# Optimization experiments

Measured on AMD Instinct MI355X. Metric: run time of the kernel, lower is better.

## Reference

```python
import jax, jax.numpy as jnp
import numpy as np

SCALE = 1.0

def _sq_dist(p0, p1):
    # p0: [B,N,3], p1: [B,M,3] -> [B,N,M] squared euclidean distances
    n0 = jnp.sum(p0 * p0, axis=-1)  # [B,N]
    n1 = jnp.sum(p1 * p1, axis=-1)  # [B,M]
    inner = jnp.einsum('bnd,bmd->bnm', p0, p1)  # [B,N,M]
    return n0[:, :, None] + n1[:, None, :] - 2.0 * inner

def setup_inputs() -> dict:
    key = jax.random.key(0)
    k0, k1 = jax.random.split(key)
    template = jax.random.normal(k0, (4, 8192, 3), dtype=jnp.float32)
    source = jax.random.normal(k1, (4, 8192, 3), dtype=jnp.float32)
    return {"template": template, "source": source}

def reference(template, source):
    p0 = template / SCALE
    p1 = source / SCALE
    d = _sq_dist(p0, p1)  # [B,N,M]
    # nearest neighbor in each direction, averaged over points
    d01 = jnp.mean(jnp.min(d, axis=2), axis=1)  # template -> source, [B]
    d10 = jnp.mean(jnp.min(d, axis=1), axis=1)  # source -> template, [B]
    return d01 + d10  # per-batch chamfer distance (reduction='none')
```

## Files before the change

kernel.cpp:

```cpp
#include <hip/hip_runtime.h>


typedef __bf16 bf16x8 __attribute__((ext_vector_type(8)));
typedef float  f32x16 __attribute__((ext_vector_type(16)));

constexpr int B     = 4;
constexpr int NPTS  = 8192;
constexpr int BLOCK = 256;
constexpr int QPW   = 64;
constexpr int QPB   = 256;
constexpr int QBLKS = NPTS / QPB;
constexpr int CH    = 4;
constexpr int CPTS  = NPTS / CH;
constexpr int SPTS  = 512;
constexpr int NPASS = CPTS / SPTS;
constexpr int TPP   = SPTS / 32;
constexpr size_t KEYBYTES = (size_t)2 * B * NPTS * sizeof(unsigned);

__device__ inline unsigned key_of(float f) {
    unsigned b = __float_as_uint(f);
    return b ^ (unsigned)(((int)b >> 31) | (int)0x80000000u);
}
__device__ inline float float_of(unsigned k) {
    unsigned b = (k & 0x80000000u) ? (k ^ 0x80000000u) : ~k;
    return __uint_as_float(b);
}

__global__ __launch_bounds__(BLOCK) void chamfer_prep(
    const float* __restrict__ tpl, const float* __restrict__ src,
    bf16x8* __restrict__ efrag)
{
    const int pt  = blockIdx.x * BLOCK + threadIdx.x;
    const int c   = blockIdx.y;
    const int b   = c & (B - 1);
    const int dir = c >> 2;
    const float* db = (dir == 0 ? src : tpl) + (size_t)b * NPTS * 3;

    float x = db[3 * pt], y = db[3 * pt + 1], z = db[3 * pt + 2];
    float n = -0.5f * (x * x + y * y + z * z);
    __bf16 hx = (__bf16)x, hy = (__bf16)y, hz = (__bf16)z;
    __bf16 lx = (__bf16)(x - (float)hx);
    __bf16 ly = (__bf16)(y - (float)hy);
    __bf16 lz = (__bf16)(z - (float)hz);
    __bf16 nh = (__bf16)n;
    __bf16 nl = (__bf16)(n - (float)nh);
    const __bf16 zb = (__bf16)0.0f;

    bf16x8 e0 = {hx, hy, hz, lx, ly, lz, hx, hy};
    bf16x8 e1 = {hz, nh, nl, lx, ly, lz, zb, zb};
    size_t base = ((size_t)c * NPTS + pt) * 2;
    efrag[base]     = e0;
    efrag[base + 1] = e1;
}

__global__ __launch_bounds__(BLOCK, 4) void chamfer_sweep(
    const float* __restrict__ tpl, const float* __restrict__ src,
    const bf16x8* __restrict__ efrag,
    unsigned* __restrict__ keys)
{
    __shared__ bf16x8 sbuf[SPTS * 2];

    const int tid = threadIdx.x;
    const int l   = tid & 63;
    const int w   = tid >> 6;
    const int h   = l >> 5;
    const int r32 = l & 31;
    const int c   = blockIdx.z;
    const int b   = c & (B - 1);
    const int dir = c >> 2;
    const float* q = (dir == 0 ? tpl : src) + (size_t)b * NPTS * 3;
    const int qbase  = blockIdx.x * QPB + w * QPW;
    const int cstart = blockIdx.y * CPTS;

    const __bf16 one = (__bf16)1.0f, zb = (__bf16)0.0f;
    bf16x8 fa[2];
    #pragma unroll
    for (int f = 0; f < 2; ++f) {
        int qi = qbase + f * 32 + r32;
        float x = q[3 * qi], y = q[3 * qi + 1], z = q[3 * qi + 2];
        __bf16 hx = (__bf16)x, hy = (__bf16)y, hz = (__bf16)z;
        __bf16 lx = (__bf16)(x - (float)hx);
        __bf16 ly = (__bf16)(y - (float)hy);
        __bf16 lz = (__bf16)(z - (float)hz);
        if (h == 0) fa[f] = (bf16x8){hx, hy, hz, hx, hy, hz, lx, ly};
        else        fa[f] = (bf16x8){lz, one, one, lx, ly, lz, zb, zb};
    }

    f32x16 best0, best1, zc;
    #pragma unroll
    for (int r = 0; r < 16; ++r) { best0[r] = -3.4e38f; best1[r] = -3.4e38f; zc[r] = 0.0f; }

    const bf16x8* eb = efrag + ((size_t)c * NPTS + cstart) * 2;
    bf16x8 rg[4];
    #pragma unroll
    for (int i = 0; i < 4; ++i) rg[i] = eb[tid + i * 256];

    for (int p = 0; p < NPASS; ++p) {
        __syncthreads();
        #pragma unroll
        for (int i = 0; i < 4; ++i) sbuf[tid + i * 256] = rg[i];
        if (p + 1 < NPASS) {
            const bf16x8* ebn = eb + (size_t)(p + 1) * SPTS * 2;
            #pragma unroll
            for (int i = 0; i < 4; ++i) rg[i] = ebn[tid + i * 256];
        }
        __syncthreads();

        #pragma unroll 2
        for (int t = 0; t < TPP; ++t) {
            bf16x8 bv = sbuf[t * 64 + r32 * 2 + h];
            f32x16 d0 = __builtin_amdgcn_mfma_f32_32x32x16_bf16(fa[0], bv, zc, 0, 0, 0);
            f32x16 d1 = __builtin_amdgcn_mfma_f32_32x32x16_bf16(fa[1], bv, zc, 0, 0, 0);
            #pragma unroll
            for (int r = 0; r < 16; ++r) {
                best0[r] = fmaxf(best0[r], d0[r]);
                best1[r] = fmaxf(best1[r], d1[r]);
            }
        }
    }

    #pragma unroll
    for (int m = 1; m < 32; m <<= 1) {
        #pragma unroll
        for (int r = 0; r < 16; ++r) {
            best0[r] = fmaxf(best0[r], __shfl_xor(best0[r], m, 64));
            best1[r] = fmaxf(best1[r], __shfl_xor(best1[r], m, 64));
        }
    }
    if (r32 == 0) {
        unsigned* kz = keys + (size_t)c * NPTS;
        #pragma unroll
        for (int r = 0; r < 16; ++r) {
            int row = (r & 3) + 8 * (r >> 2) + 4 * h;
            atomicMax(&kz[qbase + row],      key_of(best0[r]));
            atomicMax(&kz[qbase + 32 + row], key_of(best1[r]));
        }
    }
}

__global__ __launch_bounds__(256) void chamfer_final(
    const float* __restrict__ tpl, const float* __restrict__ src,
    const unsigned* __restrict__ keys, float* __restrict__ out)
{
    __shared__ float red[256];
    const int z   = blockIdx.x >> 4;
    const int seg = blockIdx.x & 15;
    const float* qc = (z < B ? tpl : src) + (size_t)(z & (B - 1)) * NPTS * 3;

    float s = 0.f;
    const int lo = seg * (NPTS / 16);
    for (int i = lo + threadIdx.x; i < lo + NPTS / 16; i += 256) {
        float md = float_of(keys[(size_t)z * NPTS + i]);
        float x = qc[3 * i], y = qc[3 * i + 1], zz = qc[3 * i + 2];
        s += fmaf(md, -2.0f, x * x + y * y + zz * zz);
    }
    red[threadIdx.x] = s;
    __syncthreads();
    #pragma unroll
    for (int off = 128; off > 0; off >>= 1) {
        if (threadIdx.x < off) red[threadIdx.x] += red[threadIdx.x + off];
        __syncthreads();
    }
    if (threadIdx.x == 0)
        atomicAdd(&out[z & (B - 1)], red[0] * (1.0f / NPTS));
}

extern "C" void kernel_launch(void* const* d_in, const int* in_sizes, int n_in,
                              void* d_out, int out_size, void* d_ws, size_t ws_size,
                              hipStream_t stream) {
    const float* tpl = (const float*)d_in[0];
    const float* src = (const float*)d_in[1];
    float* out = (float*)d_out;
    unsigned* keys = (unsigned*)d_ws;
    bf16x8* efrag  = (bf16x8*)((char*)d_ws + KEYBYTES);

    hipMemsetAsync(d_ws, 0x00, KEYBYTES, stream);
    hipMemsetAsync(d_out, 0x00, (size_t)B * sizeof(float), stream);
    chamfer_prep <<<dim3(NPTS / BLOCK, 2 * B), BLOCK, 0, stream>>>(tpl, src, efrag);
    chamfer_sweep<<<dim3(QBLKS, CH, 2 * B),    BLOCK, 0, stream>>>(tpl, src, efrag, keys);
    chamfer_final<<<B * 16 * 2, 256, 0, stream>>>(tpl, src, keys, out);
}
```

Baseline: 41.94 us.

## Double-buffer sweep LDS via async global_load_lds and fold memsets into prep

The sweep kernel now streams each pass of encoded points straight from global memory into a double-buffered LDS tile using global_load_lds. This drops the register staging copy and one of the two barriers per pass. The MFMA loop is restructured to process two tiles per iteration and chain the max reductions. The two hipMemsetAsync calls are replaced by zeroing keys and output inside the prep kernel, and the final kernel uses one block per batch-direction instead of 16 segments. The final reduction therefore runs with much less parallelism, and correctness depends on the barrier waiting for the async LDS loads.

```diff
diff --git a/kernel.cpp b/kernel.cpp
--- a/kernel.cpp
+++ b/kernel.cpp
@@ -1,4 +1,5 @@
 #include <hip/hip_runtime.h>
+#include <stdint.h>
 
 
 typedef __bf16 bf16x8 __attribute__((ext_vector_type(8)));
@@ -15,6 +16,7 @@
 constexpr int SPTS  = 512;
 constexpr int NPASS = CPTS / SPTS;
 constexpr int TPP   = SPTS / 32;
+constexpr int PASSBYTES = SPTS * 2 * 16;
 constexpr size_t KEYBYTES = (size_t)2 * B * NPTS * sizeof(unsigned);
 
 __device__ inline unsigned key_of(float f) {
@@ -26,15 +28,25 @@
     return __uint_as_float(b);
 }
 
+__device__ inline void gload_lds16(const void* g, void* l) {
+    __builtin_amdgcn_global_load_lds(
+        (const __attribute__((address_space(1))) uint32_t*)g,
+        (__attribute__((address_space(3))) uint32_t*)l, 16, 0, 0);
+}
+
 __global__ __launch_bounds__(BLOCK) void chamfer_prep(
     const float* __restrict__ tpl, const float* __restrict__ src,
-    bf16x8* __restrict__ efrag)
+    bf16x8* __restrict__ efrag,
+    unsigned* __restrict__ keys, float* __restrict__ out)
 {
     const int pt  = blockIdx.x * BLOCK + threadIdx.x;
     const int c   = blockIdx.y;
     const int b   = c & (B - 1);
     const int dir = c >> 2;
     const float* db = (dir == 0 ? src : tpl) + (size_t)b * NPTS * 3;
+
+    keys[(size_t)c * NPTS + pt] = 0u;
+    if (blockIdx.x == 0 && c == 0 && threadIdx.x < B) out[threadIdx.x] = 0.f;
 
     float x = db[3 * pt], y = db[3 * pt + 1], z = db[3 * pt + 2];
     float n = -0.5f * (x * x + y * y + z * z);
@@ -46,11 +58,9 @@
     __bf16 nl = (__bf16)(n - (float)nh);
     const __bf16 zb = (__bf16)0.0f;
 
-    bf16x8 e0 = {hx, hy, hz, lx, ly, lz, hx, hy};
-    bf16x8 e1 = {hz, nh, nl, lx, ly, lz, zb, zb};
     size_t base = ((size_t)c * NPTS + pt) * 2;
-    efrag[base]     = e0;
-    efrag[base + 1] = e1;
+    efrag[base]     = (bf16x8){hx, hy, hz, lx, ly, lz, hx, hy};
+    efrag[base + 1] = (bf16x8){hz, nh, nl, lx, ly, lz, zb, zb};
 }
 
 __global__ __launch_bounds__(BLOCK, 4) void chamfer_sweep(
@@ -58,7 +68,7 @@
     const bf16x8* __restrict__ efrag,
     unsigned* __restrict__ keys)
 {
-    __shared__ bf16x8 sbuf[SPTS * 2];
+    __shared__ bf16x8 sbuf[2][SPTS * 2];
 
     const int tid = threadIdx.x;
     const int l   = tid & 63;
@@ -69,8 +79,14 @@
     const int b   = c & (B - 1);
     const int dir = c >> 2;
     const float* q = (dir == 0 ? tpl : src) + (size_t)b * NPTS * 3;
-    const int qbase  = blockIdx.x * QPB + w * QPW;
-    const int cstart = blockIdx.y * CPTS;
+    const int qbase = blockIdx.x * QPB + w * QPW;
+    const char* eb  = (const char*)(efrag + ((size_t)c * NPTS + blockIdx.y * CPTS) * 2);
+
+    #pragma unroll
+    for (int i = 0; i < 4; ++i) {
+        int off = (w * 4 + i) * 1024;
+        gload_lds16(eb + off + l * 16, (char*)&sbuf[0][0] + off);
+    }
 
     const __bf16 one = (__bf16)1.0f, zb = (__bf16)0.0f;
     bf16x8 fa[2];
@@ -90,32 +106,33 @@
     #pragma unroll
     for (int r = 0; r < 16; ++r) { best0[r] = -3.4e38f; best1[r] = -3.4e38f; zc[r] = 0.0f; }
 
-    const bf16x8* eb = efrag + ((size_t)c * NPTS + cstart) * 2;
-    bf16x8 rg[4];
-    #pragma unroll
-    for (int i = 0; i < 4; ++i) rg[i] = eb[tid + i * 256];
-
+    const int idx = r32 * 2 + h;
     for (int p = 0; p < NPASS; ++p) {
         __syncthreads();
+        if (p + 1 < NPASS) {
+            const char* ebn = eb + (p + 1) * PASSBYTES;
+            char* dst = (char*)&sbuf[(p + 1) & 1][0];
+            #pragma unroll
+            for (int i = 0; i < 4; ++i) {
+                int off = (w * 4 + i) * 1024;
+                gload_lds16(ebn + off + l * 16, dst + off);
+            }
+        }
+        const bf16x8* sb = sbuf[p & 1];
         #pragma unroll
-        for (int i = 0; i < 4; ++i) sbuf[tid + i * 256] = rg[i];
-        if (p + 1 < NPASS) {
-            const bf16x8* ebn = eb + (size_t)(p + 1) * SPTS * 2;
+        for (int t = 0; t < TPP; t += 2) {
+            bf16x8 bv0 = sb[t * 64 + idx];
+            bf16x8 bv1 = sb[(t + 1) * 64 + idx];
+            f32x16 d00 = __builtin_amdgcn_mfma_f32_32x32x16_bf16(fa[0], bv0, zc, 0, 0, 0);
+            f32x16 d01 = __builtin_amdgcn_mfma_f32_32x32x16_bf16(fa[0], bv1, zc, 0, 0, 0);
             #pragma unroll
-            for (int i = 0; i < 4; ++i) rg[i] = ebn[tid + i * 256];
-        }
-        __syncthreads();
-
-        #pragma unroll 2
-        for (int t = 0; t < TPP; ++t) {
-            bf16x8 bv = sbuf[t * 64 + r32 * 2 + h];
-            f32x16 d0 = __builtin_amdgcn_mfma_f32_32x32x16_bf16(fa[0], bv, zc, 0, 0, 0);
-            f32x16 d1 = __builtin_amdgcn_mfma_f32_32x32x16_bf16(fa[1], bv, zc, 0, 0, 0);
+            for (int r = 0; r < 16; ++r)
+                best0[r] = fmaxf(fmaxf(best0[r], d00[r]), d01[r]);
+            f32x16 d10 = __builtin_amdgcn_mfma_f32_32x32x16_bf16(fa[1], bv0, zc, 0, 0, 0);
+            f32x16 d11 = __builtin_amdgcn_mfma_f32_32x32x16_bf16(fa[1], bv1, zc, 0, 0, 0);
             #pragma unroll
-            for (int r = 0; r < 16; ++r) {
-                best0[r] = fmaxf(best0[r], d0[r]);
-                best1[r] = fmaxf(best1[r], d1[r]);
-            }
+            for (int r = 0; r < 16; ++r)
+                best1[r] = fmaxf(fmaxf(best1[r], d10[r]), d11[r]);
         }
     }
 
@@ -143,13 +160,11 @@
     const unsigned* __restrict__ keys, float* __restrict__ out)
 {
     __shared__ float red[256];
-    const int z   = blockIdx.x >> 4;
-    const int seg = blockIdx.x & 15;
+    const int z = blockIdx.x;
     const float* qc = (z < B ? tpl : src) + (size_t)(z & (B - 1)) * NPTS * 3;
 
     float s = 0.f;
-    const int lo = seg * (NPTS / 16);
-    for (int i = lo + threadIdx.x; i < lo + NPTS / 16; i += 256) {
+    for (int i = threadIdx.x; i < NPTS; i += 256) {
         float md = float_of(keys[(size_t)z * NPTS + i]);
         float x = qc[3 * i], y = qc[3 * i + 1], zz = qc[3 * i + 2];
         s += fmaf(md, -2.0f, x * x + y * y + zz * zz);
@@ -174,9 +189,7 @@
     unsigned* keys = (unsigned*)d_ws;
     bf16x8* efrag  = (bf16x8*)((char*)d_ws + KEYBYTES);
 
-    hipMemsetAsync(d_ws, 0x00, KEYBYTES, stream);
-    hipMemsetAsync(d_out, 0x00, (size_t)B * sizeof(float), stream);
-    chamfer_prep <<<dim3(NPTS / BLOCK, 2 * B), BLOCK, 0, stream>>>(tpl, src, efrag);
+    chamfer_prep <<<dim3(NPTS / BLOCK, 2 * B), BLOCK, 0, stream>>>(tpl, src, efrag, keys, out);
     chamfer_sweep<<<dim3(QBLKS, CH, 2 * B),    BLOCK, 0, stream>>>(tpl, src, efrag, keys);
-    chamfer_final<<<B * 16 * 2, 256, 0, stream>>>(tpl, src, keys, out);
+    chamfer_final<<<2 * B, 256, 0, stream>>>(tpl, src, keys, out);
 }
```

After: 43.98 us. +4.8%, slower.
